# Performance work log

Measured on AMD Instinct MI355X. Metric: run time of the kernel, lower is better.

Reference implementation:

```python
import jax, jax.numpy as jnp
import numpy as np

EPS = 1e-5

def conv2d(x, w, stride, pad):
    return jax.lax.conv_general_dilated(
        x, w, window_strides=(stride, stride),
        padding=[(pad, pad), (pad, pad)],
        dimension_numbers=('NCHW', 'OIHW', 'NCHW'))

def batchnorm(x, gamma, beta, mean, var):
    # inference-mode BN over channel dim of NCHW
    inv = jax.lax.rsqrt(var + EPS)
    return (x - mean[None, :, None, None]) * (inv * gamma)[None, :, None, None] + beta[None, :, None, None]

def rational(x, num, den):
    # Rational activation, version A, degrees (5,4):
    #   P(x) = num0 + num1*x + ... + num5*x^5  (Horner)
    #   Q(x) = 1 + sum_{j=1..4} |den_{j-1}| * |x|^j
    p = num[5]
    for i in range(4, -1, -1):
        p = p * x + num[i]
    xa = jnp.abs(x)
    q = jnp.ones_like(x)
    pw = xa
    for j in range(4):
        q = q + jnp.abs(den[j]) * pw
        pw = pw * xa
    return p / q

def multi_variant_rationals(out, num_r, den_r, num_g, den_g, num_b, den_b):
    # channels 0::3 -> r, 1::3 -> g, 2::3 -> b, then re-interleave
    B, C, H, W = out.shape
    o = out.reshape(B, C // 3, 3, H, W)  # channel c = 3*j + k
    r = rational(o[:, :, 0], num_r, den_r)
    g = rational(o[:, :, 1], num_g, den_g)
    b = rational(o[:, :, 2], num_b, den_b)
    return jnp.stack([r, g, b], axis=2).reshape(B, C, H, W)

def setup_inputs() -> dict:
    key = jax.random.key(0)
    ks = jax.random.split(key, 12)
    B, Cin, Cout, H, W = 64, 96, 192, 56, 56
    inp = {
        'x': jax.random.normal(ks[0], (B, Cin, H, W), jnp.float32),
        'w1': jax.random.normal(ks[1], (Cout, Cin, 3, 3), jnp.float32) * 0.05,
        'gamma1': jnp.ones((Cout,), jnp.float32),
        'beta1': jnp.zeros((Cout,), jnp.float32),
        'mean1': jnp.zeros((Cout,), jnp.float32),
        'var1': jnp.ones((Cout,), jnp.float32),
        'num_r': jax.random.normal(ks[2], (6,), jnp.float32) * 0.3,
        'den_r': jax.random.normal(ks[3], (4,), jnp.float32) * 0.3,
        'num_g': jax.random.normal(ks[4], (6,), jnp.float32) * 0.3,
        'den_g': jax.random.normal(ks[5], (4,), jnp.float32) * 0.3,
        'num_b': jax.random.normal(ks[6], (6,), jnp.float32) * 0.3,
        'den_b': jax.random.normal(ks[7], (4,), jnp.float32) * 0.3,
        'w2': jax.random.normal(ks[8], (Cout, Cout, 3, 3), jnp.float32) * 0.05,
        'gamma2': jnp.ones((Cout,), jnp.float32),
        'beta2': jnp.zeros((Cout,), jnp.float32),
        'mean2': jnp.zeros((Cout,), jnp.float32),
        'var2': jnp.ones((Cout,), jnp.float32),
        'ws': jax.random.normal(ks[9], (Cout, Cin, 1, 1), jnp.float32) * 0.05,
        'gammas': jnp.ones((Cout,), jnp.float32),
        'betas': jnp.zeros((Cout,), jnp.float32),
        'means': jnp.zeros((Cout,), jnp.float32),
        'vars_': jnp.ones((Cout,), jnp.float32),
    }
    return inp

def reference(x, w1, gamma1, beta1, mean1, var1,
              num_r, den_r, num_g, den_g, num_b, den_b,
              w2, gamma2, beta2, mean2, var2,
              ws, gammas, betas, means, vars_):
    STRIDE = 2
    out = batchnorm(conv2d(x, w1, STRIDE, 1), gamma1, beta1, mean1, var1)
    out = multi_variant_rationals(out, num_r, den_r, num_g, den_g, num_b, den_b)
    out = batchnorm(conv2d(out, w2, 1, 1), gamma2, beta2, mean2, var2)
    shortcut = batchnorm(conv2d(x, ws, STRIDE, 0), gammas, betas, means, vars_)
    out = out + shortcut
    out = multi_variant_rationals(out, num_r, den_r, num_g, den_g, num_b, den_b)
    return out
```

## Files before the change

### kernel.cpp

```cpp
#include <hip/hip_runtime.h>

#define EPSBN  1e-5f
#define NBLK_A 392
#define NBLK_B 256

#define W1B_OFF 0u
#define W2B_OFF 331776u
#define WSB_OFF 995328u
#define CS_OFF  1044480u
#define XT_OFF  1048320u
#define ACT_OFF 39583488u

typedef __attribute__((ext_vector_type(8))) short bf16x8;
typedef __attribute__((ext_vector_type(4))) short bf16x4;
typedef __attribute__((ext_vector_type(4))) float f32x4;

__device__ __forceinline__ short f2bf(float f) {
    unsigned u = __float_as_uint(f);
    u += 0x7fffu + ((u >> 16) & 1u);
    return (short)(u >> 16);
}

__device__ __forceinline__ void gload16(const short* g, short* l) {
    __builtin_amdgcn_global_load_lds(
        (const __attribute__((address_space(1))) void*)g,
        (__attribute__((address_space(3))) void*)l, 16, 0, 0);
}

__device__ __forceinline__ float rational_eval(float v, const float* nm, const float* dn) {
    float p = nm[5];
    p = p * v + nm[4];
    p = p * v + nm[3];
    p = p * v + nm[2];
    p = p * v + nm[1];
    p = p * v + nm[0];
    float xa = fabsf(v);
    float q = 1.0f;
    float pw = xa;
    q += dn[0] * pw; pw *= xa;
    q += dn[1] * pw; pw *= xa;
    q += dn[2] * pw; pw *= xa;
    q += dn[3] * pw;
    float inv = __builtin_amdgcn_rcpf(q);
    inv = inv * (2.0f - q * inv);
    return p * inv;
}

__device__ __forceinline__ void sel_coeffs(int v, const float cnm[3][6], const float cdn[3][4],
                                           float nm[6], float dn[4]) {
#pragma unroll
    for (int i = 0; i < 6; i++) nm[i] = (v == 0) ? cnm[0][i] : ((v == 1) ? cnm[1][i] : cnm[2][i]);
#pragma unroll
    for (int i = 0; i < 4; i++) dn[i] = (v == 0) ? cdn[0][i] : ((v == 1) ? cdn[1][i] : cdn[2][i]);
}

extern "C" __global__ void prep_scales_kernel(
    const float* g1, const float* b1, const float* m1, const float* v1,
    const float* g2, const float* b2, const float* m2, const float* v2,
    const float* gs, const float* bs, const float* ms, const float* vs,
    float* cs)
{
    int i = threadIdx.x;
    if (i < 192) {
        float a1 = g1[i] * rsqrtf(v1[i] + EPSBN);
        float a2 = g2[i] * rsqrtf(v2[i] + EPSBN);
        float a3 = gs[i] * rsqrtf(vs[i] + EPSBN);
        cs[i]       = a1;
        cs[192 + i] = a2;
        cs[384 + i] = a3;
        cs[576 + i] = b1[i] - m1[i] * a1;
        cs[768 + i] = (b2[i] - m2[i] * a2) + (bs[i] - ms[i] * a3);
    }
}

extern "C" __global__ void prep_w_kernel(const float* __restrict__ w, const float* __restrict__ s,
                                         short* __restrict__ wb, int CI_src, int CI_dst, int KP, int total)
{
    int i = blockIdx.x * 256 + threadIdx.x;
    if (i >= total) return;
    int co = i / (CI_dst * KP);
    int r  = i - co * CI_dst * KP;
    int kpos = r / CI_dst;
    int ci = r - kpos * CI_dst;
    wb[i] = (ci < CI_src) ? f2bf(w[(co * CI_src + ci) * KP + kpos] * s[co]) : (short)0;
}

extern "C" __global__ void ring_zero_kernel(short* __restrict__ buf, int H, int C, int total)
{
    int ring = 2 * H + 2 * (H - 2);
    int i = blockIdx.x * 256 + threadIdx.x;
    if (i >= total) return;
    int c = i % C;
    int t = i / C;
    int rp = t % ring;
    int n = t / ring;
    int h, w;
    if (rp < H)           { h = 0;          w = rp; }
    else if (rp < 2 * H)  { h = H - 1;      w = rp - H; }
    else { int k = rp - 2 * H; h = (k >> 1) + 1; w = (k & 1) ? (H - 1) : 0; }
    buf[((n * H + h) * H + w) * C + c] = 0;
}

extern "C" __global__ __launch_bounds__(256)
void xpose_kernel(const float* __restrict__ x, short* __restrict__ xt)
{
    __shared__ float t[96 * 57];
    int b = blockIdx.x;
    int n = b / 56, h = b - n * 56;
    const float* src = x + n * (96 * 3136) + h * 56;
    for (int i = threadIdx.x; i < 96 * 28; i += 256) {
        int c = i / 28, w2 = i - c * 28;
        float2 v = *(const float2*)&src[c * 3136 + w2 * 2];
        t[c * 57 + w2 * 2]     = v.x;
        t[c * 57 + w2 * 2 + 1] = v.y;
    }
    __syncthreads();
    unsigned* dst = (unsigned*)(xt + (n * 56 + h) * 56 * 96);
    for (int i = threadIdx.x; i < 56 * 48; i += 256) {
        int w = i / 48, cp = i - (i / 48) * 48;
        unsigned lo = (unsigned short)f2bf(t[(2 * cp) * 57 + w]);
        unsigned hi = (unsigned short)f2bf(t[(2 * cp + 1) * 57 + w]);
        dst[w * 48 + cp] = lo | (hi << 16);
    }
}

extern "C" __global__ __launch_bounds__(512, 4)
void convA_kernel(const short* __restrict__ xt,
                  const short* __restrict__ w1b,
                  const short* __restrict__ zbuf,
                  const float* __restrict__ bias1,
                  const float* __restrict__ num_r, const float* __restrict__ den_r,
                  const float* __restrict__ num_g, const float* __restrict__ den_g,
                  const float* __restrict__ num_b, const float* __restrict__ den_b,
                  short* __restrict__ act)
{
    __shared__ short lA[2][192 * 32];
    __shared__ short lB[2][128 * 32];

    const int tid  = threadIdx.x;
    const int lane = tid & 63;
    const int wave = tid >> 6;
    const int wm = wave >> 1, wn = wave & 1;
    const int lbid = (blockIdx.x & 7) * 49 + (blockIdx.x >> 3);
    const int p0   = lbid * 128;

    const int sA = (((tid & 3) ^ ((tid >> 3) & 3))) * 8;
    const int r1 = tid >> 2;
    const int aw1a = r1 * 864 + sA;
    const int aw1b = (128 + r1) * 864 + sA;

    int xb0; bool top, left;
    {
        int p = p0 + r1;
        int n = p / 784; int pr = p - n * 784;
        int oh = pr / 28; int ow = pr - oh * 28;
        xb0 = ((n * 56 + 2 * oh) * 56 + 2 * ow) * 96 + sA;
        top = (oh == 0); left = (ow == 0);
    }

    const int l15 = lane & 15, ksl = lane >> 4;
    int ard[3], brd[4];
#pragma unroll
    for (int m = 0; m < 3; ++m) {
        int row = wm * 48 + m * 16 + l15;
        ard[m] = row * 32 + ((ksl ^ ((row >> 1) & 3)) << 3);
    }
#pragma unroll
    for (int n = 0; n < 4; ++n) {
        int row = wn * 64 + n * 16 + l15;
        brd[n] = row * 32 + ((ksl ^ ((row >> 1) & 3)) << 3);
    }

    auto stage = [&](int buf, int t) {
        int kpos = t / 3, cb = t - 3 * kpos;
        int kh = kpos / 3, kw = kpos - 3 * kh;
        gload16(&w1b[aw1a + t * 32], &lA[buf][wave * 512]);
        if (tid < 256) gload16(&w1b[aw1b + t * 32], &lA[buf][4096 + wave * 512]);
        int bko = ((kh - 1) * 56 + (kw - 1)) * 96 + cb * 32;
        const short* src = (((kh == 0) && top) || ((kw == 0) && left)) ? zbuf : &xt[xb0 + bko];
        gload16(src, &lB[buf][wave * 512]);
    };

    f32x4 acc[3][4];
#pragma unroll
    for (int m = 0; m < 3; m++)
#pragma unroll
        for (int n = 0; n < 4; n++) acc[m][n] = (f32x4){0.f, 0.f, 0.f, 0.f};

    stage(0, 0);
    int cur = 0;
    for (int t = 0; t < 27; ++t) {
        __syncthreads();
        if (t + 1 < 27) stage(cur ^ 1, t + 1);
        bf16x8 af[3];
#pragma unroll
        for (int m = 0; m < 3; ++m) af[m] = *(const bf16x8*)&lA[cur][ard[m]];
#pragma unroll
        for (int n = 0; n < 4; ++n) {
            bf16x8 bv = *(const bf16x8*)&lB[cur][brd[n]];
#pragma unroll
            for (int m = 0; m < 3; ++m)
                acc[m][n] = __builtin_amdgcn_mfma_f32_16x16x32_bf16(af[m], bv, acc[m][n], 0, 0, 0);
        }
        cur ^= 1;
    }

    float cnm[3][6], cdn[3][4];
#pragma unroll
    for (int i = 0; i < 6; i++) { cnm[0][i] = num_r[i]; cnm[1][i] = num_g[i]; cnm[2][i] = num_b[i]; }
#pragma unroll
    for (int i = 0; i < 4; i++) { cdn[0][i] = fabsf(den_r[i]); cdn[1][i] = fabsf(den_g[i]); cdn[2][i] = fabsf(den_b[i]); }

    int abase[4];
#pragma unroll
    for (int n = 0; n < 4; ++n) {
        int pp = p0 + wn * 64 + n * 16 + l15;
        int n2 = pp / 784; int r2 = pp - n2 * 784;
        int oh2 = r2 / 28; int ow2 = r2 - oh2 * 28;
        abase[n] = ((n2 * 30 + oh2 + 1) * 30 + ow2 + 1) * 192;
    }
#pragma unroll
    for (int m = 0; m < 3; ++m) {
        int cob = wm * 48 + m * 16 + (ksl << 2);
        float res[4][4];
#pragma unroll
        for (int r = 0; r < 4; ++r) {
            float nm[6], dn[4];
            sel_coeffs((cob + r) % 3, cnm, cdn, nm, dn);
            float bv = bias1[cob + r];
#pragma unroll
            for (int n = 0; n < 4; ++n)
                res[n][r] = rational_eval(acc[m][n][r] + bv, nm, dn);
        }
#pragma unroll
        for (int n = 0; n < 4; ++n) {
            bf16x4 pk;
#pragma unroll
            for (int r = 0; r < 4; ++r) pk[r] = f2bf(res[n][r]);
            *(bf16x4*)&act[abase[n] + cob] = pk;
        }
    }
}

extern "C" __global__ __launch_bounds__(512, 2)
void convB_kernel(const short* __restrict__ act,
                  const short* __restrict__ xt,
                  const short* __restrict__ w2b,
                  const short* __restrict__ wsb,
                  const float* __restrict__ bias2s,
                  const float* __restrict__ num_r, const float* __restrict__ den_r,
                  const float* __restrict__ num_g, const float* __restrict__ den_g,
                  const float* __restrict__ num_b, const float* __restrict__ den_b,
                  float* __restrict__ outp)
{
    __shared__ short patch[53248];
    __shared__ short lA[2][6144];

    const int tid  = threadIdx.x;
    const int lane = tid & 63;
    const int wave = tid >> 6;
    const int wm = wave >> 1, wn = wave & 1;
    const int img = blockIdx.x >> 2;
    const int oh0 = (blockIdx.x & 3) * 7;

    const int l15 = lane & 15, ksl = lane >> 4;

    int F0[7], F1[7], F2[7], C7[7], SCB[7], OB[7];
    bool VAL[7];
#pragma unroll
    for (int nf = 0; nf < 7; ++nf) {
        int p = wn * 112 + nf * 16 + l15;
        int orow = p / 28, ow = p - orow * 28;
        int r0 = orow;            if (r0 > 8) r0 = 8;
        int r1_ = orow + 1;       if (r1_ > 8) r1_ = 8;
        int r2_ = orow + 2;       if (r2_ > 8) r2_ = 8;
        F0[nf] = r0 * 5760 + ow * 192;
        F1[nf] = r1_ * 5760 + ow * 192;
        F2[nf] = r2_ * 5760 + ow * 192;
        C7[nf] = ow & 7;
        int ohc = oh0 + orow; if (ohc > 27) ohc = 27;
        SCB[nf] = ((img * 56 + 2 * ohc) * 56 + 2 * ow) * 96 + ksl * 8;
        OB[nf]  = img * (192 * 784) + (oh0 + orow) * 28 + ow;
        VAL[nf] = (p < 196);
    }
    int ard[3], scA[3];
#pragma unroll
    for (int m = 0; m < 3; ++m) {
        int row = wm * 48 + m * 16 + l15;
        ard[m] = row * 32 + ((ksl ^ ((row >> 1) & 3)) << 3);
        scA[m] = row * 128 + ksl * 8;
    }

    const int prow0 = (img * 30 + oh0) * 30;
#pragma unroll
    for (int j = 0; j < 13; ++j) {
        int o = (j * 512 + tid) * 8;
        if (o > 51832) o = 51832;
        int r = o / 5760;
        int rem = o - r * 5760;
        int c = rem / 192;
        int sl = (rem - c * 192) >> 3;
        const short* src = &act[(prow0 + r * 30 + c) * 192 + ((sl ^ (c & 7)) << 3)];
        gload16(src, &patch[(j * 512 + wave * 64) * 8]);
    }

    f32x4 acc[3][7];
#pragma unroll
    for (int m = 0; m < 3; m++)
#pragma unroll
        for (int nf = 0; nf < 7; nf++) acc[m][nf] = (f32x4){0.f, 0.f, 0.f, 0.f};

#pragma unroll
    for (int s = 0; s < 3; ++s) {
        bf16x8 af[3], bfv[7];
#pragma unroll
        for (int m = 0; m < 3; ++m) af[m] = *(const bf16x8*)&wsb[scA[m] + s * 32];
#pragma unroll
        for (int nf = 0; nf < 7; ++nf) bfv[nf] = *(const bf16x8*)&xt[SCB[nf] + s * 32];
#pragma unroll
        for (int m = 0; m < 3; ++m)
#pragma unroll
            for (int nf = 0; nf < 7; ++nf)
                acc[m][nf] = __builtin_amdgcn_mfma_f32_16x16x32_bf16(af[m], bfv[nf], acc[m][nf], 0, 0, 0);
    }

    auto stageA = [&](int buf, int u) {
        int kpos = u / 6, cbk = u - 6 * kpos;
        int base = kpos * 192 + cbk * 32;
        {
            int row = tid >> 2, slot = tid & 3;
            gload16(&w2b[row * 1728 + base + ((slot ^ ((row >> 1) & 3)) << 3)],
                    &lA[buf][wave * 512]);
        }
        if (tid < 256) {
            int row = 128 + (tid >> 2), slot = tid & 3;
            gload16(&w2b[row * 1728 + base + ((slot ^ ((row >> 1) & 3)) << 3)],
                    &lA[buf][4096 + wave * 512]);
        }
    };

    stageA(0, 0);
    asm volatile("s_waitcnt vmcnt(0)" ::: "memory");
    __syncthreads();

    int cur = 0;
    for (int u = 0; u < 54; ++u) {
        if (u + 1 < 54) stageA(cur ^ 1, u + 1);
        int kpos = u / 6, cbk = u - 6 * kpos;
        int kh = kpos / 3, kw = kpos - 3 * kh;
        int kwo = kw * 192;
        int sg = cbk * 4 + ksl;
        bf16x8 af[3];
#pragma unroll
        for (int m = 0; m < 3; ++m) af[m] = *(const bf16x8*)&lA[cur][ard[m]];
#pragma unroll
        for (int nf = 0; nf < 7; ++nf) {
            int Fn = (kh == 0) ? F0[nf] : ((kh == 1) ? F1[nf] : F2[nf]);
            int addr = Fn + kwo + ((sg ^ ((C7[nf] + kw) & 7)) << 3);
            bf16x8 bv = *(const bf16x8*)&patch[addr];
#pragma unroll
            for (int m = 0; m < 3; ++m)
                acc[m][nf] = __builtin_amdgcn_mfma_f32_16x16x32_bf16(af[m], bv, acc[m][nf], 0, 0, 0);
        }
        __syncthreads();
        cur ^= 1;
    }

    float cnm[3][6], cdn[3][4];
#pragma unroll
    for (int i = 0; i < 6; i++) { cnm[0][i] = num_r[i]; cnm[1][i] = num_g[i]; cnm[2][i] = num_b[i]; }
#pragma unroll
    for (int i = 0; i < 4; i++) { cdn[0][i] = fabsf(den_r[i]); cdn[1][i] = fabsf(den_g[i]); cdn[2][i] = fabsf(den_b[i]); }

#pragma unroll
    for (int m = 0; m < 3; ++m) {
        int cob = wm * 48 + m * 16 + (ksl << 2);
#pragma unroll
        for (int r = 0; r < 4; ++r) {
            float nm[6], dn[4];
            sel_coeffs((cob + r) % 3, cnm, cdn, nm, dn);
            float bv = bias2s[cob + r];
#pragma unroll
            for (int nf = 0; nf < 7; ++nf) {
                if (VAL[nf])
                    outp[OB[nf] + (cob + r) * 784] = rational_eval(acc[m][nf][r] + bv, nm, dn);
            }
        }
    }
}

extern "C" void kernel_launch(void* const* d_in, const int* in_sizes, int n_in,
                              void* d_out, int out_size, void* d_ws, size_t ws_size,
                              hipStream_t stream)
{
    const float* x      = (const float*)d_in[0];
    const float* w1     = (const float*)d_in[1];
    const float* gamma1 = (const float*)d_in[2];
    const float* beta1  = (const float*)d_in[3];
    const float* mean1  = (const float*)d_in[4];
    const float* var1   = (const float*)d_in[5];
    const float* num_r  = (const float*)d_in[6];
    const float* den_r  = (const float*)d_in[7];
    const float* num_g  = (const float*)d_in[8];
    const float* den_g  = (const float*)d_in[9];
    const float* num_b  = (const float*)d_in[10];
    const float* den_b  = (const float*)d_in[11];
    const float* w2     = (const float*)d_in[12];
    const float* gamma2 = (const float*)d_in[13];
    const float* beta2  = (const float*)d_in[14];
    const float* var2   = (const float*)d_in[16];
    const float* mean2  = (const float*)d_in[15];
    const float* wsc    = (const float*)d_in[17];
    const float* gammas = (const float*)d_in[18];
    const float* betas  = (const float*)d_in[19];
    const float* means  = (const float*)d_in[20];
    const float* vars_  = (const float*)d_in[21];

    char* base = (char*)d_ws;
    short* w1b  = (short*)(base + W1B_OFF);
    short* w2b  = (short*)(base + W2B_OFF);
    short* wsb  = (short*)(base + WSB_OFF);
    float* cs   = (float*)(base + CS_OFF);
    short* xt   = (short*)(base + XT_OFF);
    short* act  = (short*)(base + ACT_OFF);
    float* outp = (float*)d_out;

    float* bias1  = cs + 576;
    float* bias2s = cs + 768;
    const short* zbuf = wsb + 96;

    prep_scales_kernel<<<1, 256, 0, stream>>>(gamma1, beta1, mean1, var1,
                                              gamma2, beta2, mean2, var2,
                                              gammas, betas, means, vars_, cs);

    prep_w_kernel<<<(192 * 96 * 9 + 255) / 256, 256, 0, stream>>>(w1, cs, w1b, 96, 96, 9, 192 * 96 * 9);
    prep_w_kernel<<<(192 * 192 * 9 + 255) / 256, 256, 0, stream>>>(w2, cs + 192, w2b, 192, 192, 9, 192 * 192 * 9);
    prep_w_kernel<<<(192 * 128 + 255) / 256, 256, 0, stream>>>(wsc, cs + 384, wsb, 96, 128, 1, 192 * 128);

    {
        int tot_a = 64 * (2 * 30 + 2 * 28) * 192;
        ring_zero_kernel<<<(tot_a + 255) / 256, 256, 0, stream>>>(act, 30, 192, tot_a);
    }

    xpose_kernel<<<64 * 56, 256, 0, stream>>>(x, xt);

    convA_kernel<<<NBLK_A, 512, 0, stream>>>(xt, w1b, zbuf, bias1,
                                             num_r, den_r, num_g, den_g, num_b, den_b,
                                             act);

    convB_kernel<<<NBLK_B, 512, 0, stream>>>(act, xt, w2b, wsb, bias2s,
                                             num_r, den_r, num_g, den_g, num_b, den_b,
                                             outp);
}
```

Measured before the change: 154.4 us.

## Merge prep kernels and use padded-stride LDS patch in convB

Folds the scale, weight-conversion and ring-zero kernels into one launch, with each branch recomputing its BN scale inline. In convB the LDS activation patch switches from an XOR-swizzled layout filled by async global-to-LDS loads to a padded pixel stride of 196 shorts, filled by ordinary register loads and stores. This simplifies per-iteration address math and drops the per-row clamps. convB launch bounds drop to 1 block per CU and the K loop is fully unrolled, which may raise register use and change how well loads overlap with MFMA work.

```diff
diff --git a/kernel.cpp b/kernel.cpp
--- a/kernel.cpp
+++ b/kernel.cpp
@@ -3,6 +3,7 @@
 #define EPSBN  1e-5f
 #define NBLK_A 392
 #define NBLK_B 256
+#define PSTR   196
 
 #define W1B_OFF 0u
 #define W2B_OFF 331776u
@@ -54,51 +55,58 @@
     for (int i = 0; i < 4; i++) dn[i] = (v == 0) ? cdn[0][i] : ((v == 1) ? cdn[1][i] : cdn[2][i]);
 }
 
-extern "C" __global__ void prep_scales_kernel(
+extern "C" __global__ void prep_all_kernel(
+    const float* __restrict__ w1, const float* __restrict__ w2, const float* __restrict__ wsc,
     const float* g1, const float* b1, const float* m1, const float* v1,
     const float* g2, const float* b2, const float* m2, const float* v2,
     const float* gs, const float* bs, const float* ms, const float* vs,
-    float* cs)
+    short* __restrict__ w1b, short* __restrict__ w2b, short* __restrict__ wsb,
+    float* __restrict__ cs, short* __restrict__ act)
 {
-    int i = threadIdx.x;
-    if (i < 192) {
-        float a1 = g1[i] * rsqrtf(v1[i] + EPSBN);
-        float a2 = g2[i] * rsqrtf(v2[i] + EPSBN);
-        float a3 = gs[i] * rsqrtf(vs[i] + EPSBN);
-        cs[i]       = a1;
-        cs[192 + i] = a2;
-        cs[384 + i] = a3;
-        cs[576 + i] = b1[i] - m1[i] * a1;
-        cs[768 + i] = (b2[i] - m2[i] * a2) + (bs[i] - ms[i] * a3);
-    }
-}
-
-extern "C" __global__ void prep_w_kernel(const float* __restrict__ w, const float* __restrict__ s,
-                                         short* __restrict__ wb, int CI_src, int CI_dst, int KP, int total)
-{
-    int i = blockIdx.x * 256 + threadIdx.x;
-    if (i >= total) return;
-    int co = i / (CI_dst * KP);
-    int r  = i - co * CI_dst * KP;
-    int kpos = r / CI_dst;
-    int ci = r - kpos * CI_dst;
-    wb[i] = (ci < CI_src) ? f2bf(w[(co * CI_src + ci) * KP + kpos] * s[co]) : (short)0;
-}
-
-extern "C" __global__ void ring_zero_kernel(short* __restrict__ buf, int H, int C, int total)
-{
-    int ring = 2 * H + 2 * (H - 2);
-    int i = blockIdx.x * 256 + threadIdx.x;
-    if (i >= total) return;
-    int c = i % C;
-    int t = i / C;
-    int rp = t % ring;
-    int n = t / ring;
-    int h, w;
-    if (rp < H)           { h = 0;          w = rp; }
-    else if (rp < 2 * H)  { h = H - 1;      w = rp - H; }
-    else { int k = rp - 2 * H; h = (k >> 1) + 1; w = (k & 1) ? (H - 1) : 0; }
-    buf[((n * H + h) * H + w) * C + c] = 0;
+    int blk = blockIdx.x;
+    if (blk < 1296) {
+        int i = blk * 256 + threadIdx.x;
+        int co = i / 1728;
+        int r  = i - co * 1728;
+        int kpos = r / 192;
+        int ci = r - kpos * 192;
+        float a = g2[co] * rsqrtf(v2[co] + EPSBN);
+        w2b[i] = f2bf(w2[(co * 192 + ci) * 9 + kpos] * a);
+    } else if (blk < 1944) {
+        int i = (blk - 1296) * 256 + threadIdx.x;
+        int co = i / 864;
+        int r  = i - co * 864;
+        int kpos = r / 96;
+        int ci = r - kpos * 96;
+        float a = g1[co] * rsqrtf(v1[co] + EPSBN);
+        w1b[i] = f2bf(w1[(co * 96 + ci) * 9 + kpos] * a);
+    } else if (blk < 2040) {
+        int i = (blk - 1944) * 256 + threadIdx.x;
+        int co = i >> 7;
+        int ci = i & 127;
+        float a = gs[co] * rsqrtf(vs[co] + EPSBN);
+        wsb[i] = (ci < 96) ? f2bf(wsc[co * 96 + ci] * a) : (short)0;
+    } else if (blk < 7608) {
+        int i = (blk - 2040) * 256 + threadIdx.x;
+        int c = i % 192;
+        int t = i / 192;
+        int rp = t % 116;
+        int n = t / 116;
+        int h, w;
+        if (rp < 30)      { h = 0;  w = rp; }
+        else if (rp < 60) { h = 29; w = rp - 30; }
+        else { int k = rp - 60; h = (k >> 1) + 1; w = (k & 1) ? 29 : 0; }
+        act[((n * 30 + h) * 30 + w) * 192 + c] = 0;
+    } else {
+        int i = threadIdx.x;
+        if (i < 192) {
+            float a1 = g1[i] * rsqrtf(v1[i] + EPSBN);
+            float a2 = g2[i] * rsqrtf(v2[i] + EPSBN);
+            float a3 = gs[i] * rsqrtf(vs[i] + EPSBN);
+            cs[576 + i] = b1[i] - m1[i] * a1;
+            cs[768 + i] = (b2[i] - m2[i] * a2) + (bs[i] - ms[i] * a3);
+        }
+    }
 }
 
 extern "C" __global__ __launch_bounds__(256)
@@ -242,7 +250,7 @@
     }
 }
 
-extern "C" __global__ __launch_bounds__(512, 2)
+extern "C" __global__ __launch_bounds__(512, 1)
 void convB_kernel(const short* __restrict__ act,
                   const short* __restrict__ xt,
                   const short* __restrict__ w2b,
@@ -253,8 +261,8 @@
                   const float* __restrict__ num_b, const float* __restrict__ den_b,
                   float* __restrict__ outp)
 {
-    __shared__ short patch[53248];
-    __shared__ short lA[2][6144];
+    __shared__ short patch[9 * 30 * PSTR];
+    __shared__ short lA[2][192 * 32];
 
     const int tid  = threadIdx.x;
     const int lane = tid & 63;
@@ -265,20 +273,15 @@
 
     const int l15 = lane & 15, ksl = lane >> 4;
 
-    int F0[7], F1[7], F2[7], C7[7], SCB[7], OB[7];
+    int PB[7], SCB[7], OB[7];
     bool VAL[7];
 #pragma unroll
     for (int nf = 0; nf < 7; ++nf) {
         int p = wn * 112 + nf * 16 + l15;
         int orow = p / 28, ow = p - orow * 28;
-        int r0 = orow;            if (r0 > 8) r0 = 8;
-        int r1_ = orow + 1;       if (r1_ > 8) r1_ = 8;
-        int r2_ = orow + 2;       if (r2_ > 8) r2_ = 8;
-        F0[nf] = r0 * 5760 + ow * 192;
-        F1[nf] = r1_ * 5760 + ow * 192;
-        F2[nf] = r2_ * 5760 + ow * 192;
-        C7[nf] = ow & 7;
-        int ohc = oh0 + orow; if (ohc > 27) ohc = 27;
+        int orc = orow > 6 ? 6 : orow;
+        PB[nf] = (orc * 30 + ow) * PSTR + ksl * 8;
+        int ohc = oh0 + orc;
         SCB[nf] = ((img * 56 + 2 * ohc) * 56 + 2 * ow) * 96 + ksl * 8;
         OB[nf]  = img * (192 * 784) + (oh0 + orow) * 28 + ow;
         VAL[nf] = (p < 196);
@@ -293,15 +296,13 @@
 
     const int prow0 = (img * 30 + oh0) * 30;
 #pragma unroll
-    for (int j = 0; j < 13; ++j) {
-        int o = (j * 512 + tid) * 8;
-        if (o > 51832) o = 51832;
-        int r = o / 5760;
-        int rem = o - r * 5760;
-        int c = rem / 192;
-        int sl = (rem - c * 192) >> 3;
-        const short* src = &act[(prow0 + r * 30 + c) * 192 + ((sl ^ (c & 7)) << 3)];
-        gload16(src, &patch[(j * 512 + wave * 64) * 8]);
+    for (int t = 0; t < 13; ++t) {
+        int idx = t * 512 + tid;
+        if (idx < 6480) {
+            int pix = idx / 24, sl = idx - pix * 24;
+            bf16x8 v = *(const bf16x8*)&act[(prow0 + (pix / 30) * 30 + (pix % 30)) * 192 + sl * 8];
+            *(bf16x8*)&patch[pix * PSTR + sl * 8] = v;
+        }
     }
 
     f32x4 acc[3][7];
@@ -324,46 +325,42 @@
                 acc[m][nf] = __builtin_amdgcn_mfma_f32_16x16x32_bf16(af[m], bfv[nf], acc[m][nf], 0, 0, 0);
     }
 
-    auto stageA = [&](int buf, int u) {
-        int kpos = u / 6, cbk = u - 6 * kpos;
-        int base = kpos * 192 + cbk * 32;
-        {
-            int row = tid >> 2, slot = tid & 3;
-            gload16(&w2b[row * 1728 + base + ((slot ^ ((row >> 1) & 3)) << 3)],
-                    &lA[buf][wave * 512]);
-        }
-        if (tid < 256) {
-            int row = 128 + (tid >> 2), slot = tid & 3;
-            gload16(&w2b[row * 1728 + base + ((slot ^ ((row >> 1) & 3)) << 3)],
-                    &lA[buf][4096 + wave * 512]);
+    auto stageA = [&](int buf, int kw_off) {
+        if (wave < 6) {
+#pragma unroll
+            for (int j = 0; j < 2; ++j) {
+                int rg = wave * 2 + j;
+                int row = rg * 16 + (lane >> 2);
+                int sl = (lane & 3) ^ ((row >> 1) & 3);
+                gload16(&w2b[row * 1728 + kw_off + sl * 8], &lA[buf][rg * 512]);
+            }
         }
     };
 
     stageA(0, 0);
-    asm volatile("s_waitcnt vmcnt(0)" ::: "memory");
     __syncthreads();
 
-    int cur = 0;
+#pragma unroll
     for (int u = 0; u < 54; ++u) {
-        if (u + 1 < 54) stageA(cur ^ 1, u + 1);
-        int kpos = u / 6, cbk = u - 6 * kpos;
-        int kh = kpos / 3, kw = kpos - 3 * kh;
-        int kwo = kw * 192;
-        int sg = cbk * 4 + ksl;
+        const int cur = u & 1;
+        if (u + 1 < 54) {
+            const int un = u + 1, kp = un / 6, cb = un - 6 * kp;
+            stageA(cur ^ 1, kp * 192 + cb * 32);
+        }
+        const int kpos = u / 6, cbk = u - 6 * kpos;
+        const int kh = kpos / 3, kw = kpos - 3 * kh;
+        const int KOFF = (kh * 30 + kw) * PSTR + cbk * 32;
         bf16x8 af[3];
 #pragma unroll
         for (int m = 0; m < 3; ++m) af[m] = *(const bf16x8*)&lA[cur][ard[m]];
 #pragma unroll
         for (int nf = 0; nf < 7; ++nf) {
-            int Fn = (kh == 0) ? F0[nf] : ((kh == 1) ? F1[nf] : F2[nf]);
-            int addr = Fn + kwo + ((sg ^ ((C7[nf] + kw) & 7)) << 3);
-            bf16x8 bv = *(const bf16x8*)&patch[addr];
+            bf16x8 bv = *(const bf16x8*)&patch[PB[nf] + KOFF];
 #pragma unroll
             for (int m = 0; m < 3; ++m)
                 acc[m][nf] = __builtin_amdgcn_mfma_f32_16x16x32_bf16(af[m], bv, acc[m][nf], 0, 0, 0);
         }
         __syncthreads();
-        cur ^= 1;
     }
 
     float cnm[3][6], cdn[3][4];
@@ -408,8 +405,8 @@
     const float* w2     = (const float*)d_in[12];
     const float* gamma2 = (const float*)d_in[13];
     const float* beta2  = (const float*)d_in[14];
+    const float* mean2  = (const float*)d_in[15];
     const float* var2   = (const float*)d_in[16];
-    const float* mean2  = (const float*)d_in[15];
     const float* wsc    = (const float*)d_in[17];
     const float* gammas = (const float*)d_in[18];
     const float* betas  = (const float*)d_in[19];
@@ -429,18 +426,11 @@
     float* bias2s = cs + 768;
     const short* zbuf = wsb + 96;
 
-    prep_scales_kernel<<<1, 256, 0, stream>>>(gamma1, beta1, mean1, var1,
+    prep_all_kernel<<<7609, 256, 0, stream>>>(w1, w2, wsc,
+                                              gamma1, beta1, mean1, var1,
                                               gamma2, beta2, mean2, var2,
-                                              gammas, betas, means, vars_, cs);
-
-    prep_w_kernel<<<(192 * 96 * 9 + 255) / 256, 256, 0, stream>>>(w1, cs, w1b, 96, 96, 9, 192 * 96 * 9);
-    prep_w_kernel<<<(192 * 192 * 9 + 255) / 256, 256, 0, stream>>>(w2, cs + 192, w2b, 192, 192, 9, 192 * 192 * 9);
-    prep_w_kernel<<<(192 * 128 + 255) / 256, 256, 0, stream>>>(wsc, cs + 384, wsb, 96, 128, 1, 192 * 128);
-
-    {
-        int tot_a = 64 * (2 * 30 + 2 * 28) * 192;
-        ring_zero_kernel<<<(tot_a + 255) / 256, 256, 0, stream>>>(act, 30, 192, tot_a);
-    }
+                                              gammas, betas, means, vars_,
+                                              w1b, w2b, wsb, cs, act);
 
     xpose_kernel<<<64 * 56, 256, 0, stream>>>(x, xt);
 
```

After: 141.9 us. -8.1%, faster.
